# Optimization experiments

Measured on AMD Instinct MI355X. Metric: run time of the kernel, lower is better.

Reference implementation:

```python
import jax, jax.numpy as jnp
import numpy as np

NUM_HEADS = 16
HEAD_DIM = 80  # embed_dim 1280 / 16


def setup_inputs() -> dict:
    key = jax.random.key(0)
    ks = jax.random.split(key, 5)
    E = NUM_HEADS * HEAD_DIM
    sq, b = 1024, 8
    x = jax.random.normal(ks[0], (sq, b, E), dtype=jnp.float32)
    w_in = jax.random.normal(ks[1], (E, 3 * E), dtype=jnp.float32) * (E ** -0.5)
    b_in = jax.random.normal(ks[2], (3 * E,), dtype=jnp.float32) * 0.01
    w_out = jax.random.normal(ks[3], (E, E), dtype=jnp.float32) * (E ** -0.5)
    b_out = jax.random.normal(ks[4], (E,), dtype=jnp.float32) * 0.01
    return {"x": x, "w_in": w_in, "b_in": b_in, "w_out": w_out, "b_out": b_out}


def reference(x, w_in, b_in, w_out, b_out):
    sq, b, E = x.shape
    H, D = NUM_HEADS, HEAD_DIM
    norm_factor = jnp.asarray(D ** 0.5, x.dtype)
    # in_proj: [sq, b, 3E] -> [sq, b, H, 3D], split into q/k/v along last dim
    mixed = (x @ w_in + b_in).reshape(sq, b, H, 3 * D)
    q, k, v = jnp.split(mixed, 3, axis=-1)  # each [sq, b, H, D]
    # merge (b, H) and move to batch-of-bmm layout [b*H, sq, D]
    q = q.reshape(sq, b * H, D).transpose(1, 0, 2) / norm_factor
    k = k.reshape(sq, b * H, D).transpose(1, 0, 2)
    v = v.reshape(sq, b * H, D).transpose(1, 0, 2)
    scores = jnp.einsum('nqd,nkd->nqk', q, k)  # [b*H, sq, sq]
    probs = jax.nn.softmax(scores, axis=-1)
    ctx = jnp.einsum('nqk,nkd->nqd', probs, v)  # [b*H, sq, D]
    # [b, H, sq, D] -> [sq, b, H, D] -> [sq, b, E]
    ctx = ctx.reshape(b, H, sq, D).transpose(2, 0, 1, 3).reshape(sq, b, E)
    return ctx @ w_out + b_out
```

## Files before the change

kernel.cpp:

```cpp
#include <hip/hip_runtime.h>

#define DEVI __device__ __forceinline__

typedef _Float16 f16x8 __attribute__((ext_vector_type(8)));
typedef _Float16 f16x4v __attribute__((ext_vector_type(4)));
typedef _Float16 f16x2 __attribute__((ext_vector_type(2)));
typedef __fp16 fp16x2 __attribute__((ext_vector_type(2)));
typedef float f32x4 __attribute__((ext_vector_type(4)));
typedef float f32x16 __attribute__((ext_vector_type(16)));
typedef unsigned u32x4 __attribute__((ext_vector_type(4)));

DEVI void gl16(const void* g, void* l) {
  __builtin_amdgcn_global_load_lds((const __attribute__((address_space(1))) void*)g,
                                   (__attribute__((address_space(3))) void*)l, 16, 0, 0);
}

#define VMCNT(N) asm volatile("s_waitcnt vmcnt(" #N ")" ::: "memory")
#define LGKM0() asm volatile("s_waitcnt lgkmcnt(0)" ::: "memory")
#define BARRIER() asm volatile("s_barrier" ::: "memory")

DEVI unsigned pk2(float a, float b) {
  fp16x2 t = __builtin_amdgcn_cvt_pkrtz(a, b);
  return __builtin_bit_cast(unsigned, t);
}
DEVI void pl32swap(unsigned &a, unsigned &b) {
  asm volatile("v_permlane32_swap_b32 %0, %1" : "+v"(a), "+v"(b));
}

__global__ __launch_bounds__(256) void k_prep(const float* __restrict__ x, _Float16* __restrict__ xb,
                                              const float* __restrict__ w_in, _Float16* __restrict__ w_inT,
                                              const float* __restrict__ w_out, _Float16* __restrict__ w_outT) {
  __shared__ float t[32][33];
  int bid = blockIdx.x;
  int tid = threadIdx.x;
  if (bid < 2048) {
    const int n4 = 8192 * 1280 / 4;
    for (int i = bid * 256 + tid; i < n4; i += 2048 * 256) {
      float4 v = ((const float4*)x)[i];
      f16x4v h = { (_Float16)v.x, (_Float16)v.y, (_Float16)v.z, (_Float16)v.w };
      ((f16x4v*)xb)[i] = h;
    }
    return;
  }
  const float* in; _Float16* out; int R, C, tIdx; bool perm;
  if (bid < 6848) { in = w_in;  out = w_inT;  R = 1280; C = 3840; tIdx = bid - 2048; perm = true; }
  else            { in = w_out; out = w_outT; R = 1280; C = 1280; tIdx = bid - 6848; perm = false; }
  int ntc = C / 32;
  int cb = (tIdx % ntc) * 32, rb = (tIdx / ntc) * 32;
  int tx = tid & 31, ty = tid >> 5;
  #pragma unroll
  for (int i = ty; i < 32; i += 8) t[i][tx] = in[(size_t)(rb + i) * C + cb + tx];
  __syncthreads();
  #pragma unroll
  for (int i = ty; i < 32; i += 8) {
    int c = cb + i;
    if (perm) {
      int hq = c / 240, tt = c - hq * 240;
      int reg = tt / 80, d = tt - reg * 80;
      c = reg * 1280 + hq * 80 + d;
    }
    out[(size_t)c * R + rb + tx] = (_Float16)t[tx][i];
  }
}


#define MM(NLO, AF, BF) do {                                                                       \
    __builtin_amdgcn_s_setprio(1);                                                                 \
    _Pragma("unroll")                                                                              \
    for (int m_ = 0; m_ < 8; m_++) {                                                               \
      acc[m_][NLO]     = __builtin_amdgcn_mfma_f32_16x16x32_f16(AF[m_], BF[NLO],     acc[m_][NLO],     0, 0, 0); \
      acc[m_][NLO + 1] = __builtin_amdgcn_mfma_f32_16x16x32_f16(AF[m_], BF[NLO + 1], acc[m_][NLO + 1], 0, 0, 0); \
    }                                                                                              \
    __builtin_amdgcn_s_setprio(0);                                                                 \
  } while (0)

#define LDA(KT, KK, DST) do {                                                                      \
    const _Float16* bas_ = &smem[(size_t)((((KT) & 1) * 2) + wr) * 8192];                          \
    _Pragma("unroll")                                                                              \
    for (int m_ = 0; m_ < 8; m_++)                                                                 \
      DST[m_] = *(const f16x8*)&bas_[(m_ * 16 + ln) * 64 + (((((KK) * 4) + g) ^ chB) << 3)];       \
  } while (0)

#define LDB(KT, KK, DST) do {                                                                      \
    const _Float16* bas_ = &smem[32768 + (size_t)((((KT) & 1) * 2) + (wc >> 1)) * 8192];           \
    _Pragma("unroll")                                                                              \
    for (int n_ = 0; n_ < 4; n_++)                                                                 \
      DST[n_] = *(const f16x8*)&bas_[((wc & 1) * 64 + n_ * 16 + ln) * 64 + (((((KK) * 4) + g) ^ chB) << 3)]; \
  } while (0)

template<int M, int N, int K>
__global__ __launch_bounds__(512, 2) void k_gemm8(const _Float16* __restrict__ A, const _Float16* __restrict__ BT,
                                                  const float* __restrict__ bias,
                                                  _Float16* __restrict__ qo, _Float16* __restrict__ ko,
                                                  _Float16* __restrict__ vo) {
  extern __shared__ _Float16 smem[];
  constexpr int NT = K / 64;
  constexpr int NI = NT / 2;
  const int tid = threadIdx.x;
  const int w = tid >> 6, lane = tid & 63, ln = lane & 15, g = lane >> 4;
  const int wr = w >> 2, wc = w & 3;
  const int l8 = lane >> 3, l7 = lane & 7;
  const int stChunk = (l7 ^ l8) << 3;
  const int chB = ln & 7;

  constexpr int MT = M / 256;
  const int xcd = blockIdx.x & 7;
  const int i = blockIdx.x >> 3;
  const int bm0 = (xcd * (MT / 8) + (i & 3)) * 256;
  const int bn0 = (i >> 2) * 256;

  auto stgA = [&](int kt, int hh) {
    _Float16* ldsb = &smem[(size_t)((kt & 1) * 2 + hh) * 8192 + w * 1024];
    const _Float16* g0 = &A[(size_t)(bm0 + hh * 128 + w * 16 + l8) * K + kt * 64 + stChunk];
    gl16(g0, ldsb);
    gl16(g0 + (size_t)8 * K, ldsb + 512);
  };
  auto stgB = [&](int kt, int hh) {
    _Float16* ldsb = &smem[32768 + (size_t)((kt & 1) * 2 + hh) * 8192 + w * 1024];
    const _Float16* g0 = &BT[(size_t)(bn0 + hh * 128 + w * 16 + l8) * K + kt * 64 + stChunk];
    gl16(g0, ldsb);
    gl16(g0 + (size_t)8 * K, ldsb + 512);
  };

  f32x4 acc[8][4] = {};
  f16x8 a0[8], a1[8], b0[4], b1[4];

  stgB(0, 0); stgB(0, 1); stgA(0, 0); stgA(0, 1);
  stgB(1, 0); stgB(1, 1); stgA(1, 0);
  VMCNT(6);
  BARRIER();
  LDA(0, 0, a0); LDB(0, 0, b0);

  for (int it = 0; it < NI; ++it) {
    const int T0 = 2 * it, T1 = 2 * it + 1;
    const int S0 = (T0 + 2 < NT) ? T0 + 2 : 0;
    const int S1 = (T1 + 2 < NT) ? T1 + 2 : 1;
    LDB(T0, 1, b1);
    stgA(T1, 1);
    BARRIER();
    MM(0, a0, b0);
    LGKM0(); BARRIER();
    LDA(T0, 1, a1);
    stgB(S0, 0);
    BARRIER();
    MM(2, a0, b0);
    LGKM0(); BARRIER();
    stgB(S0, 1);
    BARRIER();
    MM(0, a1, b1);
    VMCNT(4);
    LGKM0(); BARRIER();
    LDA(T1, 0, a0); LDB(T1, 0, b0);
    stgA(S0, 0);
    BARRIER();
    MM(2, a1, b1);
    LGKM0(); BARRIER();
    LDB(T1, 1, b1);
    stgA(S0, 1);
    BARRIER();
    MM(0, a0, b0);
    LGKM0(); BARRIER();
    LDA(T1, 1, a1);
    stgB(S1, 0);
    BARRIER();
    MM(2, a0, b0);
    LGKM0(); BARRIER();
    stgB(S1, 1);
    BARRIER();
    MM(0, a1, b1);
    VMCNT(4);
    LGKM0(); BARRIER();
    LDA(S0, 0, a0); LDB(S0, 0, b0);
    stgA(S1, 0);
    BARRIER();
    MM(2, a1, b1);
    LGKM0(); BARRIER();
  }

  VMCNT(0);
  BARRIER();
  _Float16* sH = smem;
  const int regn = bn0 / 1280;
  const int relb = bn0 - regn * 1280;
  #pragma unroll
  for (int n = 0; n < 4; n++) {
    int col = wc * 64 + n * 16 + ln;
    int rel = relb + col;
    int h = rel / 80, d = rel - h * 80;
    float bv = bias[h * 240 + regn * 80 + d];
    float scl = (regn == 0) ? (0.11180339887498948f * 1.4426950408889634f) : 1.0f;
    #pragma unroll
    for (int m = 0; m < 8; m++) {
      #pragma unroll
      for (int r = 0; r < 4; r++) {
        int row = wr * 128 + m * 16 + 4 * g + r;
        sH[row * 256 + col] = (_Float16)((acc[m][n][r] + bv) * scl);
      }
    }
  }
  LGKM0();
  BARRIER();
  _Float16* dst = (regn == 0) ? qo : (regn == 1) ? ko : vo;
  #pragma unroll
  for (int i2 = 0; i2 < 16; i2++) {
    int id = tid + 512 * i2;
    int row = id >> 5, c8 = id & 31;
    f16x8 v = *(const f16x8*)&sH[row * 256 + c8 * 8];
    int rel = relb + c8 * 8;
    int h = rel / 80, d0 = rel - h * 80;
    int grow = bm0 + row;
    *(f16x8*)&dst[(size_t)(((grow & 7) * 16 + h) * 1024 + (grow >> 3)) * 80 + d0] = v;
  }
}


#define MMo(NLO, AF, BF) do {                                                                      \
    __builtin_amdgcn_s_setprio(1);                                                                 \
    _Pragma("unroll")                                                                              \
    for (int m_ = 0; m_ < 4; m_++) {                                                               \
      acc[m_][NLO]     = __builtin_amdgcn_mfma_f32_16x16x32_f16(AF[m_], BF[NLO],     acc[m_][NLO],     0, 0, 0); \
      acc[m_][NLO + 1] = __builtin_amdgcn_mfma_f32_16x16x32_f16(AF[m_], BF[NLO + 1], acc[m_][NLO + 1], 0, 0, 0); \
    }                                                                                              \
    __builtin_amdgcn_s_setprio(0);                                                                 \
  } while (0)

#define LDAo(KT, KK, DST) do {                                                                     \
    const _Float16* bas_ = &smem[(size_t)((KT) & 1) * 8192];                                       \
    _Pragma("unroll")                                                                              \
    for (int m_ = 0; m_ < 4; m_++)                                                                 \
      DST[m_] = *(const f16x8*)&bas_[(wr * 64 + m_ * 16 + ln) * 64 + (((((KK) * 4) + g) ^ chB) << 3)]; \
  } while (0)

#define LDBo(KT, KK, DST) do {                                                                     \
    const _Float16* bas_ = &smem[16384 + (size_t)(((KT) & 1) * 2 + (wc >> 1)) * 8192];             \
    _Pragma("unroll")                                                                              \
    for (int n_ = 0; n_ < 4; n_++)                                                                 \
      DST[n_] = *(const f16x8*)&bas_[((wc & 1) * 64 + n_ * 16 + ln) * 64 + (((((KK) * 4) + g) ^ chB) << 3)]; \
  } while (0)

template<int M, int N, int K>
__global__ __launch_bounds__(512, 2) void k_gemm8o(const _Float16* __restrict__ A, const _Float16* __restrict__ BT,
                                                   const float* __restrict__ bias, float* __restrict__ outF) {
  extern __shared__ _Float16 smem[];
  constexpr int NT = K / 64;
  constexpr int NI = NT / 2;
  const int tid = threadIdx.x;
  const int w = tid >> 6, lane = tid & 63, ln = lane & 15, g = lane >> 4;
  const int wr = w >> 2, wc = w & 3;
  const int l8 = lane >> 3, l7 = lane & 7;
  const int stChunk = (l7 ^ l8) << 3;
  const int chB = ln & 7;

  const int xcd = blockIdx.x & 7;
  const int i = blockIdx.x >> 3;
  const int bm0 = (xcd * 8 + (i & 7)) * 128;
  const int bn0 = (i >> 3) * 256;

  auto stgA = [&](int kt) {
    _Float16* ldsb = &smem[(size_t)(kt & 1) * 8192 + w * 1024];
    const _Float16* g0 = &A[(size_t)(bm0 + w * 16 + l8) * K + kt * 64 + stChunk];
    gl16(g0, ldsb);
    gl16(g0 + (size_t)8 * K, ldsb + 512);
  };
  auto stgB = [&](int kt, int hh) {
    _Float16* ldsb = &smem[16384 + (size_t)((kt & 1) * 2 + hh) * 8192 + w * 1024];
    const _Float16* g0 = &BT[(size_t)(bn0 + hh * 128 + w * 16 + l8) * K + kt * 64 + stChunk];
    gl16(g0, ldsb);
    gl16(g0 + (size_t)8 * K, ldsb + 512);
  };

  f32x4 acc[4][4] = {};
  f16x8 a0[4], a1[4], b0[4], b1[4];

  stgB(0, 0); stgB(0, 1); stgA(0);
  stgB(1, 0); stgB(1, 1); stgA(1);
  VMCNT(6);
  BARRIER();
  LDAo(0, 0, a0); LDBo(0, 0, b0);

  for (int it = 0; it < NI; ++it) {
    const int T0 = 2 * it, T1 = 2 * it + 1;
    const int S0 = (T0 + 2 < NT) ? T0 + 2 : 0;
    const int S1 = (T1 + 2 < NT) ? T1 + 2 : 1;
    LDBo(T0, 1, b1);
    BARRIER(); MMo(0, a0, b0); LGKM0(); BARRIER();
    LDAo(T0, 1, a1);
    stgB(S0, 0);
    BARRIER(); MMo(2, a0, b0); LGKM0(); BARRIER();
    stgB(S0, 1);
    BARRIER(); MMo(0, a1, b1); VMCNT(4); LGKM0(); BARRIER();
    LDAo(T1, 0, a0); LDBo(T1, 0, b0);
    stgA(S0);
    BARRIER(); MMo(2, a1, b1); LGKM0(); BARRIER();
    LDBo(T1, 1, b1);
    BARRIER(); MMo(0, a0, b0); LGKM0(); BARRIER();
    LDAo(T1, 1, a1);
    stgB(S1, 0);
    BARRIER(); MMo(2, a0, b0); LGKM0(); BARRIER();
    stgB(S1, 1);
    BARRIER(); MMo(0, a1, b1); VMCNT(4); LGKM0(); BARRIER();
    LDAo(S0, 0, a0); LDBo(S0, 0, b0);
    stgA(S1);
    BARRIER(); MMo(2, a1, b1); LGKM0(); BARRIER();
  }

  VMCNT(0);
  #pragma unroll
  for (int n = 0; n < 4; n++) {
    int col = bn0 + wc * 64 + n * 16 + ln;
    float bv = bias[col];
    #pragma unroll
    for (int m = 0; m < 4; m++) {
      int rbase = bm0 + wr * 64 + m * 16 + 4 * g;
      #pragma unroll
      for (int r = 0; r < 4; r++)
        outF[(size_t)(rbase + r) * N + col] = acc[m][n][r] + bv;
    }
  }
}

__global__ __launch_bounds__(512, 2) void k_attn(const _Float16* __restrict__ qb, const _Float16* __restrict__ kb,
                                                 const _Float16* __restrict__ vb, _Float16* __restrict__ ctxg) {
  extern __shared__ _Float16 smem[];
  _Float16* Kb0 = smem;
  _Float16* Kb1 = smem + 8192;
  _Float16* Vb0 = smem + 16384;
  _Float16* Vb1 = smem + 16384 + 6144;

  const int tid = threadIdx.x;
  const int w = tid >> 6, lane = tid & 63;
  const int l32 = lane & 31, h = lane >> 5;
  const int lx = l32 & 7;
  const int xcd = blockIdx.x & 7;
  const int j = blockIdx.x >> 3;
  const int head = xcd + 8 * (j & 15);
  const int s0 = (j >> 4) * 256;
  const int bb = head >> 4, h16 = head & 15;
  const size_t hbase = (size_t)head * 81920;

  const int cA = tid;
  const int cB = (tid < 128) ? tid + 512 : tid;
  const int sA = cA & 63, dA = cA >> 6;
  const int sB = cB & 63, dB = cB >> 6;
  const _Float16* kGA = kb + hbase + sA * 80 + dA * 8;
  const _Float16* kGB = kb + hbase + sB * 80 + dB * 8;
  const int kOA = sA * 128 + ((dA ^ (sA & 7)) << 3);
  const int kOB = sB * 128 + ((dB ^ (sB & 7)) << 3);

  const int s4 = tid & 15, dc = tid >> 4;
  const _Float16* vG = vb + hbase + (s4 * 4) * 80 + dc * 8;

  uint4 krA, krB, vq0, vq1, vq2, vq3;
  auto issue = [&](int kt) {
    krA = *(const uint4*)(kGA + kt * 5120);
    krB = *(const uint4*)(kGB + kt * 5120);
    if (tid < 160) {
      const _Float16* p = vG + kt * 5120;
      vq0 = *(const uint4*)(p);
      vq1 = *(const uint4*)(p + 80);
      vq2 = *(const uint4*)(p + 160);
      vq3 = *(const uint4*)(p + 240);
    }
  };
  auto stage = [&](int b) {
    _Float16* kd = b ? Kb1 : Kb0;
    _Float16* vd = b ? Vb1 : Vb0;
    *(uint4*)(kd + kOA) = krA;
    *(uint4*)(kd + kOB) = krB;
    if (tid < 160) {
      const unsigned* w0 = (const unsigned*)&vq0;
      const unsigned* w1 = (const unsigned*)&vq1;
      const unsigned* w2 = (const unsigned*)&vq2;
      const unsigned* w3 = (const unsigned*)&vq3;
      #pragma unroll
      for (int jj = 0; jj < 8; ++jj) {
        int jw = jj >> 1;
        unsigned lo, hi;
        if (jj & 1) {
          lo = (w0[jw] >> 16) | (w1[jw] & 0xffff0000u);
          hi = (w2[jw] >> 16) | (w3[jw] & 0xffff0000u);
        } else {
          lo = (w0[jw] & 0xffffu) | (w1[jw] << 16);
          hi = (w2[jw] & 0xffffu) | (w3[jw] << 16);
        }
        unsigned long long u = (unsigned long long)lo | ((unsigned long long)hi << 32);
        int d = dc * 8 + jj;
        *(unsigned long long*)(vd + d * 64 + (((s4 >> 1) ^ jj) << 3) + ((s4 & 1) << 2)) = u;
      }
    }
  };

  const int qrow = s0 + w * 32 + l32;
  f16x8 qf[5];
  #pragma unroll
  for (int s = 0; s < 5; s++)
    qf[s] = *(const f16x8*)&qb[(size_t)(head * 1024 + qrow) * 80 + s * 16 + h * 8];

  f32x16 ct[3] = {};
  float m_run = -INFINITY;

  issue(0);
  stage(0);
  if (tid < 64) {
    Vb0[80 * 64 + tid] = (_Float16)1.0f;
    Vb1[80 * 64 + tid] = (_Float16)1.0f;
  }
  LGKM0();
  BARRIER();
  issue(1);

  for (int kt = 0; kt < 16; ++kt) {
    const _Float16* kc = (kt & 1) ? Kb1 : Kb0;
    const _Float16* vc = (kt & 1) ? Vb1 : Vb0;

    f32x16 sc0 = {}, sc1 = {};
    __builtin_amdgcn_s_setprio(1);
    #pragma unroll
    for (int s = 0; s < 5; ++s) {
      f16x8 kf0 = *(const f16x8*)&kc[l32 * 128 + (((2 * s + h) ^ lx) << 3)];
      f16x8 kf1 = *(const f16x8*)&kc[(32 + l32) * 128 + (((2 * s + h) ^ lx) << 3)];
      sc0 = __builtin_amdgcn_mfma_f32_32x32x16_f16(kf0, qf[s], sc0, 0, 0, 0);
      sc1 = __builtin_amdgcn_mfma_f32_32x32x16_f16(kf1, qf[s], sc1, 0, 0, 0);
    }
    __builtin_amdgcn_s_setprio(0);

    float mx[8];
    #pragma unroll
    for (int i = 0; i < 8; ++i)
      mx[i] = fmaxf(fmaxf(sc0[i], sc0[i + 8]), fmaxf(sc1[i], sc1[i + 8]));
    #pragma unroll
    for (int i = 0; i < 4; ++i) mx[i] = fmaxf(mx[i], mx[i + 4]);
    float tm = fmaxf(fmaxf(mx[0], mx[2]), fmaxf(mx[1], mx[3]));
    tm = fmaxf(tm, __shfl_xor(tm, 32));

    if (__any(tm > m_run + 8.f)) {
      float mnew = fmaxf(m_run, tm);
      float fac = exp2f(m_run - mnew);
      #pragma unroll
      for (int dt = 0; dt < 3; ++dt)
        #pragma unroll
        for (int i = 0; i < 16; ++i) ct[dt][i] *= fac;
      m_run = mnew;
    }

    float p0[16], p1[16];
    #pragma unroll
    for (int i = 0; i < 16; ++i) p0[i] = exp2f(sc0[i] - m_run);
    #pragma unroll
    for (int i = 0; i < 16; ++i) p1[i] = exp2f(sc1[i] - m_run);

    unsigned fr[4][4];
    #define PACK4(T, PP) do {                                                \
        _Pragma("unroll")                                                    \
        for (int s16 = 0; s16 < 2; ++s16) {                                  \
          unsigned u0 = pk2(PP[8 * s16 + 0], PP[8 * s16 + 1]);               \
          unsigned u1 = pk2(PP[8 * s16 + 2], PP[8 * s16 + 3]);               \
          unsigned u2 = pk2(PP[8 * s16 + 4], PP[8 * s16 + 5]);               \
          unsigned u3 = pk2(PP[8 * s16 + 6], PP[8 * s16 + 7]);               \
          pl32swap(u0, u2); pl32swap(u1, u3);                                \
          fr[2 * (T) + s16][0] = u0; fr[2 * (T) + s16][1] = u1;              \
          fr[2 * (T) + s16][2] = u2; fr[2 * (T) + s16][3] = u3;              \
        }                                                                    \
      } while (0)
    PACK4(0, p0);
    PACK4(1, p1);

    __builtin_amdgcn_s_setprio(1);
    #pragma unroll
    for (int ss = 0; ss < 4; ++ss) {
      u32x4 fu = { fr[ss][0], fr[ss][1], fr[ss][2], fr[ss][3] };
      f16x8 pf = __builtin_bit_cast(f16x8, fu);
      #pragma unroll
      for (int dt = 0; dt < 3; ++dt) {
        f16x8 vf = *(const f16x8*)&vc[(dt * 32 + l32) * 64 + (((2 * ss + h) ^ lx) << 3)];
        ct[dt] = __builtin_amdgcn_mfma_f32_32x32x16_f16(vf, pf, ct[dt], 0, 0, 0);
      }
    }
    __builtin_amdgcn_s_setprio(0);

    if (kt < 15) {
      stage((kt + 1) & 1);
      LGKM0();
      BARRIER();
      if (kt < 14) issue(kt + 2);
    }
  }

  float lsum = __shfl(ct[2][8], l32);
  float inv = 1.f / lsum;
  int sq = s0 + w * 32 + l32;
  _Float16* outp = ctxg + (size_t)(sq * 8 + bb) * 1280 + h16 * 80 + 4 * h;
  #pragma unroll
  for (int dt = 0; dt < 3; ++dt)
    #pragma unroll
    for (int rq = 0; rq < 4; ++rq) {
      if (dt == 2 && rq >= 2) continue;
      f16x4v o = { (_Float16)(ct[dt][rq * 4 + 0] * inv), (_Float16)(ct[dt][rq * 4 + 1] * inv),
                   (_Float16)(ct[dt][rq * 4 + 2] * inv), (_Float16)(ct[dt][rq * 4 + 3] * inv) };
      *(f16x4v*)&outp[dt * 32 + rq * 8] = o;
    }
}

extern "C" void kernel_launch(void* const* d_in, const int* in_sizes, int n_in,
                              void* d_out, int out_size, void* d_ws, size_t ws_size,
                              hipStream_t stream) {
  const float* x     = (const float*)d_in[0];
  const float* w_in  = (const float*)d_in[1];
  const float* b_in  = (const float*)d_in[2];
  const float* w_out = (const float*)d_in[3];
  const float* b_out = (const float*)d_in[4];
  float* out = (float*)d_out;

  char* ws = (char*)d_ws;
  size_t off = 0;
  auto carve = [&](size_t bytes) -> void* {
    void* p = ws + off;
    off += (bytes + 255) & ~(size_t)255;
    return p;
  };
  _Float16* xb     = (_Float16*)carve(8192ull * 1280 * 2);
  _Float16* w_inT  = (_Float16*)carve(3840ull * 1280 * 2);
  _Float16* w_outT = (_Float16*)carve(1280ull * 1280 * 2);
  _Float16* qb     = (_Float16*)carve(128ull * 1024 * 80 * 2);
  _Float16* kbuf   = (_Float16*)carve(128ull * 1024 * 80 * 2);
  _Float16* vbuf   = (_Float16*)carve(128ull * 1024 * 80 * 2);
  _Float16* ctxg   = (_Float16*)carve(8192ull * 1280 * 2);
  if (off > ws_size) return;

  hipFuncSetAttribute(reinterpret_cast<const void*>(&k_gemm8<8192, 3840, 1280>),
                      hipFuncAttributeMaxDynamicSharedMemorySize, 131072);
  hipFuncSetAttribute(reinterpret_cast<const void*>(&k_gemm8o<8192, 1280, 1280>),
                      hipFuncAttributeMaxDynamicSharedMemorySize, 98304);
  hipFuncSetAttribute(reinterpret_cast<const void*>(&k_attn),
                      hipFuncAttributeMaxDynamicSharedMemorySize, 57344);

  k_prep<<<8448, 256, 0, stream>>>(x, xb, w_in, w_inT, w_out, w_outT);

  k_gemm8<8192, 3840, 1280><<<480, 512, 131072, stream>>>(xb, w_inT, b_in, qb, kbuf, vbuf);
  k_attn<<<512, 512, 57344, stream>>>(qb, kbuf, vbuf, ctxg);
  k_gemm8o<8192, 1280, 1280><<<320, 512, 98304, stream>>>(ctxg, w_outT, b_out, out);
}
```

Measured before the change: 244.1 us.

## Replace both projection GEMMs with a unified 128x128-tile, 256-thread double-buffered kernel

Both the QKV input projection and the output projection now use one templated GEMM kernel with 128x128 tiles, 4 waves, and a plain double-buffered K loop. The previous hand-interleaved 256x256 and 128x256 ping-pong schedules are dropped. The aim is more blocks, higher occupancy (4 blocks per CU) and less scheduling complexity. In exchange it gives up the larger tile's operand reuse and the fine-grained overlap of loads with MFMA work, so each output now costs more global and LDS traffic.

```diff
diff --git a/kernel.cpp b/kernel.cpp
--- a/kernel.cpp
+++ b/kernel.cpp
@@ -64,257 +64,126 @@
 }
 
 
-#define MM(NLO, AF, BF) do {                                                                       \
-    __builtin_amdgcn_s_setprio(1);                                                                 \
-    _Pragma("unroll")                                                                              \
-    for (int m_ = 0; m_ < 8; m_++) {                                                               \
-      acc[m_][NLO]     = __builtin_amdgcn_mfma_f32_16x16x32_f16(AF[m_], BF[NLO],     acc[m_][NLO],     0, 0, 0); \
-      acc[m_][NLO + 1] = __builtin_amdgcn_mfma_f32_16x16x32_f16(AF[m_], BF[NLO + 1], acc[m_][NLO + 1], 0, 0, 0); \
-    }                                                                                              \
-    __builtin_amdgcn_s_setprio(0);                                                                 \
-  } while (0)
-
-#define LDA(KT, KK, DST) do {                                                                      \
-    const _Float16* bas_ = &smem[(size_t)((((KT) & 1) * 2) + wr) * 8192];                          \
-    _Pragma("unroll")                                                                              \
-    for (int m_ = 0; m_ < 8; m_++)                                                                 \
-      DST[m_] = *(const f16x8*)&bas_[(m_ * 16 + ln) * 64 + (((((KK) * 4) + g) ^ chB) << 3)];       \
-  } while (0)
-
-#define LDB(KT, KK, DST) do {                                                                      \
-    const _Float16* bas_ = &smem[32768 + (size_t)((((KT) & 1) * 2) + (wc >> 1)) * 8192];           \
-    _Pragma("unroll")                                                                              \
-    for (int n_ = 0; n_ < 4; n_++)                                                                 \
-      DST[n_] = *(const f16x8*)&bas_[((wc & 1) * 64 + n_ * 16 + ln) * 64 + (((((KK) * 4) + g) ^ chB) << 3)]; \
-  } while (0)
-
-template<int M, int N, int K>
-__global__ __launch_bounds__(512, 2) void k_gemm8(const _Float16* __restrict__ A, const _Float16* __restrict__ BT,
-                                                  const float* __restrict__ bias,
-                                                  _Float16* __restrict__ qo, _Float16* __restrict__ ko,
-                                                  _Float16* __restrict__ vo) {
-  extern __shared__ _Float16 smem[];
-  constexpr int NT = K / 64;
-  constexpr int NI = NT / 2;
-  const int tid = threadIdx.x;
-  const int w = tid >> 6, lane = tid & 63, ln = lane & 15, g = lane >> 4;
-  const int wr = w >> 2, wc = w & 3;
-  const int l8 = lane >> 3, l7 = lane & 7;
-  const int stChunk = (l7 ^ l8) << 3;
-  const int chB = ln & 7;
-
-  constexpr int MT = M / 256;
-  const int xcd = blockIdx.x & 7;
-  const int i = blockIdx.x >> 3;
-  const int bm0 = (xcd * (MT / 8) + (i & 3)) * 256;
-  const int bn0 = (i >> 2) * 256;
-
-  auto stgA = [&](int kt, int hh) {
-    _Float16* ldsb = &smem[(size_t)((kt & 1) * 2 + hh) * 8192 + w * 1024];
-    const _Float16* g0 = &A[(size_t)(bm0 + hh * 128 + w * 16 + l8) * K + kt * 64 + stChunk];
-    gl16(g0, ldsb);
-    gl16(g0 + (size_t)8 * K, ldsb + 512);
-  };
-  auto stgB = [&](int kt, int hh) {
-    _Float16* ldsb = &smem[32768 + (size_t)((kt & 1) * 2 + hh) * 8192 + w * 1024];
-    const _Float16* g0 = &BT[(size_t)(bn0 + hh * 128 + w * 16 + l8) * K + kt * 64 + stChunk];
-    gl16(g0, ldsb);
-    gl16(g0 + (size_t)8 * K, ldsb + 512);
-  };
-
-  f32x4 acc[8][4] = {};
-  f16x8 a0[8], a1[8], b0[4], b1[4];
-
-  stgB(0, 0); stgB(0, 1); stgA(0, 0); stgA(0, 1);
-  stgB(1, 0); stgB(1, 1); stgA(1, 0);
-  VMCNT(6);
-  BARRIER();
-  LDA(0, 0, a0); LDB(0, 0, b0);
-
-  for (int it = 0; it < NI; ++it) {
-    const int T0 = 2 * it, T1 = 2 * it + 1;
-    const int S0 = (T0 + 2 < NT) ? T0 + 2 : 0;
-    const int S1 = (T1 + 2 < NT) ? T1 + 2 : 1;
-    LDB(T0, 1, b1);
-    stgA(T1, 1);
-    BARRIER();
-    MM(0, a0, b0);
-    LGKM0(); BARRIER();
-    LDA(T0, 1, a1);
-    stgB(S0, 0);
-    BARRIER();
-    MM(2, a0, b0);
-    LGKM0(); BARRIER();
-    stgB(S0, 1);
-    BARRIER();
-    MM(0, a1, b1);
-    VMCNT(4);
-    LGKM0(); BARRIER();
-    LDA(T1, 0, a0); LDB(T1, 0, b0);
-    stgA(S0, 0);
-    BARRIER();
-    MM(2, a1, b1);
-    LGKM0(); BARRIER();
-    LDB(T1, 1, b1);
-    stgA(S0, 1);
-    BARRIER();
-    MM(0, a0, b0);
-    LGKM0(); BARRIER();
-    LDA(T1, 1, a1);
-    stgB(S1, 0);
-    BARRIER();
-    MM(2, a0, b0);
-    LGKM0(); BARRIER();
-    stgB(S1, 1);
-    BARRIER();
-    MM(0, a1, b1);
-    VMCNT(4);
-    LGKM0(); BARRIER();
-    LDA(S0, 0, a0); LDB(S0, 0, b0);
-    stgA(S1, 0);
-    BARRIER();
-    MM(2, a1, b1);
-    LGKM0(); BARRIER();
-  }
-
-  VMCNT(0);
-  BARRIER();
-  _Float16* sH = smem;
-  const int regn = bn0 / 1280;
-  const int relb = bn0 - regn * 1280;
-  #pragma unroll
-  for (int n = 0; n < 4; n++) {
-    int col = wc * 64 + n * 16 + ln;
-    int rel = relb + col;
-    int h = rel / 80, d = rel - h * 80;
-    float bv = bias[h * 240 + regn * 80 + d];
-    float scl = (regn == 0) ? (0.11180339887498948f * 1.4426950408889634f) : 1.0f;
-    #pragma unroll
-    for (int m = 0; m < 8; m++) {
-      #pragma unroll
-      for (int r = 0; r < 4; r++) {
-        int row = wr * 128 + m * 16 + 4 * g + r;
-        sH[row * 256 + col] = (_Float16)((acc[m][n][r] + bv) * scl);
-      }
-    }
-  }
-  LGKM0();
-  BARRIER();
-  _Float16* dst = (regn == 0) ? qo : (regn == 1) ? ko : vo;
-  #pragma unroll
-  for (int i2 = 0; i2 < 16; i2++) {
-    int id = tid + 512 * i2;
-    int row = id >> 5, c8 = id & 31;
-    f16x8 v = *(const f16x8*)&sH[row * 256 + c8 * 8];
-    int rel = relb + c8 * 8;
-    int h = rel / 80, d0 = rel - h * 80;
-    int grow = bm0 + row;
-    *(f16x8*)&dst[(size_t)(((grow & 7) * 16 + h) * 1024 + (grow >> 3)) * 80 + d0] = v;
-  }
-}
-
-
-#define MMo(NLO, AF, BF) do {                                                                      \
-    __builtin_amdgcn_s_setprio(1);                                                                 \
-    _Pragma("unroll")                                                                              \
-    for (int m_ = 0; m_ < 4; m_++) {                                                               \
-      acc[m_][NLO]     = __builtin_amdgcn_mfma_f32_16x16x32_f16(AF[m_], BF[NLO],     acc[m_][NLO],     0, 0, 0); \
-      acc[m_][NLO + 1] = __builtin_amdgcn_mfma_f32_16x16x32_f16(AF[m_], BF[NLO + 1], acc[m_][NLO + 1], 0, 0, 0); \
-    }                                                                                              \
-    __builtin_amdgcn_s_setprio(0);                                                                 \
-  } while (0)
-
-#define LDAo(KT, KK, DST) do {                                                                     \
-    const _Float16* bas_ = &smem[(size_t)((KT) & 1) * 8192];                                       \
+#define LDA1(BUF, KK, DST) do {                                                                    \
+    const _Float16* bas_ = &smem[(size_t)(BUF) * 8192];                                            \
     _Pragma("unroll")                                                                              \
     for (int m_ = 0; m_ < 4; m_++)                                                                 \
       DST[m_] = *(const f16x8*)&bas_[(wr * 64 + m_ * 16 + ln) * 64 + (((((KK) * 4) + g) ^ chB) << 3)]; \
   } while (0)
 
-#define LDBo(KT, KK, DST) do {                                                                     \
-    const _Float16* bas_ = &smem[16384 + (size_t)(((KT) & 1) * 2 + (wc >> 1)) * 8192];             \
+#define LDB1(BUF, KK, DST) do {                                                                    \
+    const _Float16* bas_ = &smem[16384 + (size_t)(BUF) * 8192];                                    \
     _Pragma("unroll")                                                                              \
     for (int n_ = 0; n_ < 4; n_++)                                                                 \
-      DST[n_] = *(const f16x8*)&bas_[((wc & 1) * 64 + n_ * 16 + ln) * 64 + (((((KK) * 4) + g) ^ chB) << 3)]; \
+      DST[n_] = *(const f16x8*)&bas_[(wc * 64 + n_ * 16 + ln) * 64 + (((((KK) * 4) + g) ^ chB) << 3)]; \
   } while (0)
 
-template<int M, int N, int K>
-__global__ __launch_bounds__(512, 2) void k_gemm8o(const _Float16* __restrict__ A, const _Float16* __restrict__ BT,
-                                                   const float* __restrict__ bias, float* __restrict__ outF) {
+#define MM16(AF, BF) do {                                                                          \
+    __builtin_amdgcn_s_setprio(1);                                                                 \
+    _Pragma("unroll")                                                                              \
+    for (int m_ = 0; m_ < 4; m_++)                                                                 \
+      _Pragma("unroll")                                                                            \
+      for (int n_ = 0; n_ < 4; n_++)                                                               \
+        acc[m_][n_] = __builtin_amdgcn_mfma_f32_16x16x32_f16(AF[m_], BF[n_], acc[m_][n_], 0, 0, 0);\
+    __builtin_amdgcn_s_setprio(0);                                                                 \
+  } while (0)
+
+template<int M, int N, int K, int EPI>
+__global__ __launch_bounds__(256, 4) void k_t128(const _Float16* __restrict__ A, const _Float16* __restrict__ BT,
+                                                 const float* __restrict__ bias,
+                                                 _Float16* __restrict__ qo, _Float16* __restrict__ ko,
+                                                 _Float16* __restrict__ vo, float* __restrict__ outF) {
   extern __shared__ _Float16 smem[];
   constexpr int NT = K / 64;
-  constexpr int NI = NT / 2;
   const int tid = threadIdx.x;
   const int w = tid >> 6, lane = tid & 63, ln = lane & 15, g = lane >> 4;
-  const int wr = w >> 2, wc = w & 3;
+  const int wr = w >> 1, wc = w & 1;
   const int l8 = lane >> 3, l7 = lane & 7;
   const int stChunk = (l7 ^ l8) << 3;
   const int chB = ln & 7;
 
+  constexpr int MT = M / 128, MB = MT / 8;
   const int xcd = blockIdx.x & 7;
   const int i = blockIdx.x >> 3;
-  const int bm0 = (xcd * 8 + (i & 7)) * 128;
-  const int bn0 = (i >> 3) * 256;
-
-  auto stgA = [&](int kt) {
-    _Float16* ldsb = &smem[(size_t)(kt & 1) * 8192 + w * 1024];
-    const _Float16* g0 = &A[(size_t)(bm0 + w * 16 + l8) * K + kt * 64 + stChunk];
-    gl16(g0, ldsb);
-    gl16(g0 + (size_t)8 * K, ldsb + 512);
+  const int bm0 = (xcd * MB + i % MB) * 128;
+  const int bn0 = (i / MB) * 128;
+
+  auto stage = [&](int kt) {
+    const int buf = kt & 1;
+    #pragma unroll
+    for (int sub = 0; sub < 4; ++sub) {
+      int row = w * 32 + sub * 8 + l8;
+      gl16(&A[(size_t)(bm0 + row) * K + kt * 64 + stChunk],
+           smem + (size_t)buf * 8192 + (w * 32 + sub * 8) * 64);
+      gl16(&BT[(size_t)(bn0 + row) * K + kt * 64 + stChunk],
+           smem + 16384 + (size_t)buf * 8192 + (w * 32 + sub * 8) * 64);
+    }
   };
-  auto stgB = [&](int kt, int hh) {
-    _Float16* ldsb = &smem[16384 + (size_t)((kt & 1) * 2 + hh) * 8192 + w * 1024];
-    const _Float16* g0 = &BT[(size_t)(bn0 + hh * 128 + w * 16 + l8) * K + kt * 64 + stChunk];
-    gl16(g0, ldsb);
-    gl16(g0 + (size_t)8 * K, ldsb + 512);
-  };
 
   f32x4 acc[4][4] = {};
-  f16x8 a0[4], a1[4], b0[4], b1[4];
-
-  stgB(0, 0); stgB(0, 1); stgA(0);
-  stgB(1, 0); stgB(1, 1); stgA(1);
-  VMCNT(6);
-  BARRIER();
-  LDAo(0, 0, a0); LDBo(0, 0, b0);
-
-  for (int it = 0; it < NI; ++it) {
-    const int T0 = 2 * it, T1 = 2 * it + 1;
-    const int S0 = (T0 + 2 < NT) ? T0 + 2 : 0;
-    const int S1 = (T1 + 2 < NT) ? T1 + 2 : 1;
-    LDBo(T0, 1, b1);
-    BARRIER(); MMo(0, a0, b0); LGKM0(); BARRIER();
-    LDAo(T0, 1, a1);
-    stgB(S0, 0);
-    BARRIER(); MMo(2, a0, b0); LGKM0(); BARRIER();
-    stgB(S0, 1);
-    BARRIER(); MMo(0, a1, b1); VMCNT(4); LGKM0(); BARRIER();
-    LDAo(T1, 0, a0); LDBo(T1, 0, b0);
-    stgA(S0);
-    BARRIER(); MMo(2, a1, b1); LGKM0(); BARRIER();
-    LDBo(T1, 1, b1);
-    BARRIER(); MMo(0, a0, b0); LGKM0(); BARRIER();
-    LDAo(T1, 1, a1);
-    stgB(S1, 0);
-    BARRIER(); MMo(2, a0, b0); LGKM0(); BARRIER();
-    stgB(S1, 1);
-    BARRIER(); MMo(0, a1, b1); VMCNT(4); LGKM0(); BARRIER();
-    LDAo(S0, 0, a0); LDBo(S0, 0, b0);
-    stgA(S1);
-    BARRIER(); MMo(2, a1, b1); LGKM0(); BARRIER();
-  }
-
-  VMCNT(0);
-  #pragma unroll
-  for (int n = 0; n < 4; n++) {
-    int col = bn0 + wc * 64 + n * 16 + ln;
-    float bv = bias[col];
-    #pragma unroll
-    for (int m = 0; m < 4; m++) {
-      int rbase = bm0 + wr * 64 + m * 16 + 4 * g;
+  f16x8 af[4], bf[4];
+
+  stage(0);
+  for (int kt = 0; kt < NT; ++kt) {
+    stage(kt + 1 < NT ? kt + 1 : 0);
+    VMCNT(8);
+    BARRIER();
+    const int buf = kt & 1;
+    LDA1(buf, 0, af); LDB1(buf, 0, bf);
+    MM16(af, bf);
+    LDA1(buf, 1, af); LDB1(buf, 1, bf);
+    MM16(af, bf);
+    BARRIER();
+  }
+
+  if (EPI == 1) {
+    VMCNT(0);
+    BARRIER();
+    _Float16* sH = smem;
+    const int regn = bn0 / 1280;
+    const int relb = bn0 - regn * 1280;
+    #pragma unroll
+    for (int n = 0; n < 4; n++) {
+      int col = wc * 64 + n * 16 + ln;
+      int rel = relb + col;
+      int h = rel / 80, d = rel - h * 80;
+      float bv = bias[h * 240 + regn * 80 + d];
+      float scl = (regn == 0) ? (0.11180339887498948f * 1.4426950408889634f) : 1.0f;
       #pragma unroll
-      for (int r = 0; r < 4; r++)
-        outF[(size_t)(rbase + r) * N + col] = acc[m][n][r] + bv;
+      for (int m = 0; m < 4; m++) {
+        #pragma unroll
+        for (int r = 0; r < 4; r++) {
+          int row = wr * 64 + m * 16 + 4 * g + r;
+          sH[row * 128 + col] = (_Float16)((acc[m][n][r] + bv) * scl);
+        }
+      }
+    }
+    LGKM0();
+    BARRIER();
+    _Float16* dst = (regn == 0) ? qo : (regn == 1) ? ko : vo;
+    #pragma unroll
+    for (int i2 = 0; i2 < 8; i2++) {
+      int id = tid + 256 * i2;
+      int row = id >> 4, c8 = id & 15;
+      f16x8 v = *(const f16x8*)&sH[row * 128 + c8 * 8];
+      int rel = relb + c8 * 8;
+      int h = rel / 80, d0 = rel - h * 80;
+      int grow = bm0 + row;
+      *(f16x8*)&dst[(size_t)(((grow & 7) * 16 + h) * 1024 + (grow >> 3)) * 80 + d0] = v;
+    }
+  } else {
+    VMCNT(0);
+    #pragma unroll
+    for (int n = 0; n < 4; n++) {
+      int col = bn0 + wc * 64 + n * 16 + ln;
+      float bv = bias[col];
+      #pragma unroll
+      for (int m = 0; m < 4; m++) {
+        int rbase = bm0 + wr * 64 + m * 16 + 4 * g;
+        #pragma unroll
+        for (int r = 0; r < 4; r++)
+          outF[(size_t)(rbase + r) * N + col] = acc[m][n][r] + bv;
+      }
     }
   }
 }
@@ -527,16 +396,16 @@
   _Float16* ctxg   = (_Float16*)carve(8192ull * 1280 * 2);
   if (off > ws_size) return;
 
-  hipFuncSetAttribute(reinterpret_cast<const void*>(&k_gemm8<8192, 3840, 1280>),
-                      hipFuncAttributeMaxDynamicSharedMemorySize, 131072);
-  hipFuncSetAttribute(reinterpret_cast<const void*>(&k_gemm8o<8192, 1280, 1280>),
-                      hipFuncAttributeMaxDynamicSharedMemorySize, 98304);
+  hipFuncSetAttribute(reinterpret_cast<const void*>(&k_t128<8192, 3840, 1280, 1>),
+                      hipFuncAttributeMaxDynamicSharedMemorySize, 65536);
+  hipFuncSetAttribute(reinterpret_cast<const void*>(&k_t128<8192, 1280, 1280, 0>),
+                      hipFuncAttributeMaxDynamicSharedMemorySize, 65536);
   hipFuncSetAttribute(reinterpret_cast<const void*>(&k_attn),
                       hipFuncAttributeMaxDynamicSharedMemorySize, 57344);
 
   k_prep<<<8448, 256, 0, stream>>>(x, xb, w_in, w_inT, w_out, w_outT);
 
-  k_gemm8<8192, 3840, 1280><<<480, 512, 131072, stream>>>(xb, w_inT, b_in, qb, kbuf, vbuf);
+  k_t128<8192, 3840, 1280, 1><<<1920, 256, 65536, stream>>>(xb, w_inT, b_in, qb, kbuf, vbuf, nullptr);
   k_attn<<<512, 512, 57344, stream>>>(qb, kbuf, vbuf, ctxg);
-  k_gemm8o<8192, 1280, 1280><<<320, 512, 98304, stream>>>(ctxg, w_outT, b_out, out);
-}
+  k_t128<8192, 1280, 1280, 0><<<640, 256, 65536, stream>>>(ctxg, w_outT, b_out, nullptr, nullptr, nullptr, out);
+}
```

Result: slower. 257.3 us (+5.4%).
